# Optimization experiments

Measured on AMD Instinct MI355X. Metric: run time of the kernel, lower is better.

The kernel has to match this reference:

```python
import jax, jax.numpy as jnp
import numpy as np

B, T, I, H = 4096, 512, 3, 64


def setup_inputs() -> dict:
    key = jax.random.key(0)
    ks = jax.random.split(key, 8)
    s = 1.0 / np.sqrt(H)  # PyTorch LSTM init scale
    x = jax.random.normal(ks[0], (B, T, I), dtype=jnp.float32)
    W_ih = jax.random.uniform(ks[1], (4 * H, I), minval=-s, maxval=s, dtype=jnp.float32)
    W_hh = jax.random.uniform(ks[2], (4 * H, H), minval=-s, maxval=s, dtype=jnp.float32)
    b_ih = jax.random.uniform(ks[3], (4 * H,), minval=-s, maxval=s, dtype=jnp.float32)
    b_hh = jax.random.uniform(ks[4], (4 * H,), minval=-s, maxval=s, dtype=jnp.float32)
    W_dec = jax.random.uniform(ks[5], (I, H), minval=-s, maxval=s, dtype=jnp.float32)
    b_dec = jax.random.uniform(ks[6], (I,), minval=-s, maxval=s, dtype=jnp.float32)
    return {"x": x, "W_ih": W_ih, "W_hh": W_hh, "b_ih": b_ih, "b_hh": b_hh,
            "W_dec": W_dec, "b_dec": b_dec}


def _lstm(x, W_ih, W_hh, b_ih, b_hh):
    # Precompute input contribution for all timesteps: [B, T, 4H]
    x_gates = jnp.einsum('bti,gi->btg', x, W_ih) + b_ih + b_hh
    h0 = jnp.zeros((x.shape[0], H), dtype=x.dtype)
    c0 = jnp.zeros((x.shape[0], H), dtype=x.dtype)

    def step(carry, xg_t):
        h, c = carry
        gates = xg_t + h @ W_hh.T  # [B, 4H]
        i_g, f_g, g_g, o_g = jnp.split(gates, 4, axis=-1)  # PyTorch order i,f,g,o
        i_g = jax.nn.sigmoid(i_g)
        f_g = jax.nn.sigmoid(f_g)
        g_g = jnp.tanh(g_g)
        o_g = jax.nn.sigmoid(o_g)
        c_new = f_g * c + i_g * g_g
        h_new = o_g * jnp.tanh(c_new)
        return (h_new, c_new), h_new

    _, hs = jax.lax.scan(step, (h0, c0), jnp.swapaxes(x_gates, 0, 1))  # [T, B, H]
    return jnp.swapaxes(hs, 0, 1)  # [B, T, H]


def reference(x, W_ih, W_hh, b_ih, b_hh, W_dec, b_dec):
    lstm_out = _lstm(x, W_ih, W_hh, b_ih, b_hh)
    return jnp.einsum('bth,oh->bto', lstm_out, W_dec) + b_dec  # [B, T, I]
```

## Files before the change

### kernel.cpp

```cpp
#include <hip/hip_runtime.h>


#define TLEN 512
#define TCHUNK 64
#define ROWS 16

typedef float    float4_t __attribute__((ext_vector_type(4)));
typedef _Float16 halfx8   __attribute__((ext_vector_type(8)));

#define INV2048 4.8828125e-4f

__device__ __forceinline__ float fexp2(float x){ return __builtin_amdgcn_exp2f(x); }
__device__ __forceinline__ float frcp (float x){ return __builtin_amdgcn_rcpf(x); }
__device__ __forceinline__ float sigm (float x){ return frcp(1.f + fexp2(-1.44269504f*x)); }
__device__ __forceinline__ float tanh_(float x){ return 1.f - 2.f*frcp(1.f + fexp2(2.88539008f*x)); }

__device__ __forceinline__ unsigned short hbits(_Float16 h){
  union { _Float16 h; unsigned short u; } x; x.h = h; return x.u;
}

__device__ __forceinline__ void split8h(const float* v, halfx8& hi, halfx8& lo){
  #pragma unroll
  for (int j = 0; j < 8; j++){
    _Float16 h = (_Float16)v[j];
    hi[j] = h;
    lo[j] = (_Float16)((v[j] - (float)h) * 2048.0f);
  }
}

#define MFMA(a,b,c) __builtin_amdgcn_mfma_f32_16x16x32_f16((a),(b),(c),0,0,0)

#define HHI 0
#define HS_SZ 2304
#define XOF 0
#define XPK 3136
#define OOF 7232
#define LF_SZ 10368

__global__ __launch_bounds__(256, 1)
void LSTMAnomalyDetector_kernel(
    const float* __restrict__ x,     const float* __restrict__ W_ih,
    const float* __restrict__ W_hh,  const float* __restrict__ b_ih,
    const float* __restrict__ b_hh,  const float* __restrict__ W_dec,
    const float* __restrict__ b_dec, float* __restrict__ out)
{
  __shared__ __align__(16) unsigned short HS[HS_SZ];
  __shared__ __align__(16) float          LF[LF_SZ];

  const int tid  = threadIdx.x;
  const int w    = tid >> 6;
  const int lane = tid & 63;
  const int q    = lane >> 4;
  const int lid  = lane & 15;
  const int b0   = blockIdx.x * ROWS;
  const int cw   = w*16 + lid;

  halfx8 Bh[4][2], Bl[4][2];
  halfx8 Dh[2],    Dl[2];
  float  wi[4][3], bsum[4];

  #pragma unroll
  for (int tl = 0; tl < 4; tl++){
    const int g = tl*64 + cw;
    #pragma unroll
    for (int kt = 0; kt < 2; kt++){
      const float* p = W_hh + g*64 + kt*32 + q*8;
      float v[8];
      #pragma unroll
      for (int j = 0; j < 8; j++) v[j] = p[j];
      split8h(v, Bh[tl][kt], Bl[tl][kt]);
    }
    wi[tl][0] = W_ih[g*3+0];
    wi[tl][1] = W_ih[g*3+1];
    wi[tl][2] = W_ih[g*3+2];
    bsum[tl]  = b_ih[g] + b_hh[g];
  }
  #pragma unroll
  for (int kt = 0; kt < 2; kt++){
    float v[8] = {0.f,0.f,0.f,0.f,0.f,0.f,0.f,0.f};
    if (lid < 3){
      const float* p = W_dec + lid*64 + kt*32 + q*8;
      #pragma unroll
      for (int j = 0; j < 8; j++) v[j] = p[j];
    }
    split8h(v, Dh[kt], Dl[kt]);
  }
  const float bdec = (lid < 3) ? b_dec[lid] : 0.f;

  halfx8 ah0 = {}, ah1 = {};
  float creg[4] = {0.f, 0.f, 0.f, 0.f};
  float4_t xp4[4];

  auto loadx = [&](int d){
    #pragma unroll
    for (int r = 0; r < 4; r++){
      float4_t xv = *(const float4_t*)&LF[XPK + d*64 + (q*4+r)*4];
      #pragma unroll
      for (int tl = 0; tl < 4; tl++)
        xp4[tl][r] = fmaf(wi[tl][2], xv[2],
                      fmaf(wi[tl][1], xv[1],
                        fmaf(wi[tl][0], xv[0], bsum[tl])));
    }
  };

  #pragma unroll
  for (int s = 0; s < 3; s++){
    const int f = tid + 256*s;
    const int row = f/48; const int off = (f%48)*4;
    float4_t v = *(const float4_t*)(x + (size_t)(b0+row)*1536 + off);
    *(float4_t*)&LF[XOF + row*196 + off] = v;
  }
  __syncthreads();
  #pragma unroll
  for (int s = 0; s < 4; s++){
    const int p = tid + 256*s;
    const float* xr = &LF[XOF + (p & 15)*196 + (p >> 4)*3];
    float4_t v = {xr[0], xr[1], xr[2], 0.f};
    *(float4_t*)&LF[XPK + p*4] = v;
  }
  __syncthreads();
  loadx(0);

  for (int t = 0; t < TLEN; ++t){
    const int dt = t & (TCHUNK-1);
    const int hb = (t & 1) * 1152;

    float4_t c1 = xp4[0];
    c1 = MFMA(ah0, Bh[0][0], c1);
    c1 = MFMA(ah1, Bh[0][1], c1);
    float4_t c2 = {0.f,0.f,0.f,0.f};
    c2 = MFMA(ah0, Bl[0][0], c2);
    c2 = MFMA(ah1, Bl[0][1], c2);
    float4_t g0;
    #pragma unroll
    for (int r = 0; r < 4; r++) g0[r] = fmaf(c2[r], INV2048, c1[r]);
    float4_t ig;
    #pragma unroll
    for (int r = 0; r < 4; r++) ig[r] = sigm(g0[r]);

    c1 = xp4[1];
    c1 = MFMA(ah0, Bh[1][0], c1);
    c1 = MFMA(ah1, Bh[1][1], c1);
    c2 = (float4_t){0.f,0.f,0.f,0.f};
    c2 = MFMA(ah0, Bl[1][0], c2);
    c2 = MFMA(ah1, Bl[1][1], c2);
    float4_t g1;
    #pragma unroll
    for (int r = 0; r < 4; r++) g1[r] = fmaf(c2[r], INV2048, c1[r]);
    float4_t fg;
    #pragma unroll
    for (int r = 0; r < 4; r++) fg[r] = sigm(g1[r]);

    c1 = xp4[2];
    c1 = MFMA(ah0, Bh[2][0], c1);
    c1 = MFMA(ah1, Bh[2][1], c1);
    c2 = (float4_t){0.f,0.f,0.f,0.f};
    c2 = MFMA(ah0, Bl[2][0], c2);
    c2 = MFMA(ah1, Bl[2][1], c2);
    float4_t g2;
    #pragma unroll
    for (int r = 0; r < 4; r++) g2[r] = fmaf(c2[r], INV2048, c1[r]);
    float4_t gg;
    #pragma unroll
    for (int r = 0; r < 4; r++) gg[r] = tanh_(g2[r]);

    c1 = xp4[3];
    c1 = MFMA(ah0, Bh[3][0], c1);
    c1 = MFMA(ah1, Bh[3][1], c1);
    c2 = (float4_t){0.f,0.f,0.f,0.f};
    c2 = MFMA(ah0, Bl[3][0], c2);
    c2 = MFMA(ah1, Bl[3][1], c2);
    float4_t g3;
    #pragma unroll
    for (int r = 0; r < 4; r++) g3[r] = fmaf(c2[r], INV2048, c1[r]);

    #pragma unroll
    for (int r = 0; r < 4; r++){
      const float og = sigm(g3[r]);
      creg[r] = fg[r]*creg[r] + ig[r]*gg[r];
      const float h = og * tanh_(creg[r]);
      const _Float16 h16 = (_Float16)h;
      const int m = q*4 + r;
      HS[HHI + hb + m*72 + cw] = hbits(h16);
    }

    if (dt != TCHUNK-1) loadx(dt+1);

    __syncthreads();

    {
      const unsigned short* ph = &HS[HHI + hb + lid*72 + q*8];
      ah0 = *(const halfx8*)&ph[0];
      ah1 = *(const halfx8*)&ph[32];
    }

    if (w == 0){
      float4_t d1 = {0.f,0.f,0.f,0.f};
      d1 = MFMA(ah0, Dh[0], d1);
      d1 = MFMA(ah1, Dh[1], d1);
      float4_t d2 = {0.f,0.f,0.f,0.f};
      d2 = MFMA(ah0, Dl[0], d2);
      d2 = MFMA(ah1, Dl[1], d2);
      if (lid < 3){
        #pragma unroll
        for (int r = 0; r < 4; r++)
          LF[OOF + (q*4+r)*196 + dt*3 + lid] = fmaf(d2[r], INV2048, d1[r]) + bdec;
      }
    }

    if (dt == TCHUNK-1){
      __syncthreads();
      const int t0 = t - (TCHUNK-1);
      #pragma unroll
      for (int s = 0; s < 3; s++){
        const int f = tid + 256*s;
        const int row = f/48; const int off = (f%48)*4;
        float4_t v = *(const float4_t*)&LF[OOF + row*196 + off];
        *(float4_t*)(out + (size_t)(b0+row)*1536 + t0*3 + off) = v;
      }
      if (t + 1 < TLEN){
        #pragma unroll
        for (int s = 0; s < 3; s++){
          const int f = tid + 256*s;
          const int row = f/48; const int off = (f%48)*4;
          float4_t v = *(const float4_t*)(x + (size_t)(b0+row)*1536 + (t+1)*3 + off);
          *(float4_t*)&LF[XOF + row*196 + off] = v;
        }
        __syncthreads();
        #pragma unroll
        for (int s = 0; s < 4; s++){
          const int p = tid + 256*s;
          const float* xr = &LF[XOF + (p & 15)*196 + (p >> 4)*3];
          float4_t v = {xr[0], xr[1], xr[2], 0.f};
          *(float4_t*)&LF[XPK + p*4] = v;
        }
      }
      __syncthreads();
      if (t + 1 < TLEN) loadx(0);
    }
  }
}

extern "C" void kernel_launch(void* const* d_in, const int* in_sizes, int n_in,
                              void* d_out, int out_size, void* d_ws, size_t ws_size,
                              hipStream_t stream)
{
  const float* x     = (const float*)d_in[0];
  const float* W_ih  = (const float*)d_in[1];
  const float* W_hh  = (const float*)d_in[2];
  const float* b_ih  = (const float*)d_in[3];
  const float* b_hh  = (const float*)d_in[4];
  const float* W_dec = (const float*)d_in[5];
  const float* b_dec = (const float*)d_in[6];
  float* out = (float*)d_out;

  const int B = in_sizes[0] / (TLEN * 3);
  const int blocks = B / ROWS;
  hipLaunchKernelGGL(LSTMAnomalyDetector_kernel, dim3(blocks), dim3(256), 0, stream,
                     x, W_ih, W_hh, b_ih, b_hh, W_dec, b_dec, out);
}
```

Baseline: 485.3 us.

## Rotate decoder MFMA across waves, defer it into next step, drop lo-split

Result: no change. 492.1 us (+1.4%).

```diff
diff --git a/kernel.cpp b/kernel.cpp
--- a/kernel.cpp
+++ b/kernel.cpp
@@ -56,7 +56,7 @@
   const int cw   = w*16 + lid;
 
   halfx8 Bh[4][2], Bl[4][2];
-  halfx8 Dh[2],    Dl[2];
+  halfx8 Dh[2];
   float  wi[4][3], bsum[4];
 
   #pragma unroll
@@ -77,13 +77,13 @@
   }
   #pragma unroll
   for (int kt = 0; kt < 2; kt++){
-    float v[8] = {0.f,0.f,0.f,0.f,0.f,0.f,0.f,0.f};
+    #pragma unroll
+    for (int j = 0; j < 8; j++) Dh[kt][j] = (_Float16)0.f;
     if (lid < 3){
       const float* p = W_dec + lid*64 + kt*32 + q*8;
       #pragma unroll
-      for (int j = 0; j < 8; j++) v[j] = p[j];
-    }
-    split8h(v, Dh[kt], Dl[kt]);
+      for (int j = 0; j < 8; j++) Dh[kt][j] = (_Float16)p[j];
+    }
   }
   const float bdec = (lid < 3) ? b_dec[lid] : 0.f;
 
@@ -138,6 +138,18 @@
     #pragma unroll
     for (int r = 0; r < 4; r++) ig[r] = sigm(g0[r]);
 
+    if (t > 0 && w == ((t-1) & 3)){
+      float4_t d1 = {0.f,0.f,0.f,0.f};
+      d1 = MFMA(ah0, Dh[0], d1);
+      d1 = MFMA(ah1, Dh[1], d1);
+      if (lid < 3){
+        const int dto = (t-1) & (TCHUNK-1);
+        #pragma unroll
+        for (int r = 0; r < 4; r++)
+          LF[OOF + (q*4+r)*196 + dto*3 + lid] = d1[r] + bdec;
+      }
+    }
+
     c1 = xp4[1];
     c1 = MFMA(ah0, Bh[1][0], c1);
     c1 = MFMA(ah1, Bh[1][1], c1);
@@ -194,23 +206,8 @@
       ah1 = *(const halfx8*)&ph[32];
     }
 
-    if (w == 0){
-      float4_t d1 = {0.f,0.f,0.f,0.f};
-      d1 = MFMA(ah0, Dh[0], d1);
-      d1 = MFMA(ah1, Dh[1], d1);
-      float4_t d2 = {0.f,0.f,0.f,0.f};
-      d2 = MFMA(ah0, Dl[0], d2);
-      d2 = MFMA(ah1, Dl[1], d2);
-      if (lid < 3){
-        #pragma unroll
-        for (int r = 0; r < 4; r++)
-          LF[OOF + (q*4+r)*196 + dt*3 + lid] = fmaf(d2[r], INV2048, d1[r]) + bdec;
-      }
-    }
-
-    if (dt == TCHUNK-1){
-      __syncthreads();
-      const int t0 = t - (TCHUNK-1);
+    if (dt == 0 && t > 0){
+      const int t0 = t - TCHUNK;
       #pragma unroll
       for (int s = 0; s < 3; s++){
         const int f = tid + 256*s;
@@ -218,25 +215,49 @@
         float4_t v = *(const float4_t*)&LF[OOF + row*196 + off];
         *(float4_t*)(out + (size_t)(b0+row)*1536 + t0*3 + off) = v;
       }
-      if (t + 1 < TLEN){
-        #pragma unroll
-        for (int s = 0; s < 3; s++){
-          const int f = tid + 256*s;
-          const int row = f/48; const int off = (f%48)*4;
-          float4_t v = *(const float4_t*)(x + (size_t)(b0+row)*1536 + (t+1)*3 + off);
-          *(float4_t*)&LF[XOF + row*196 + off] = v;
-        }
-        __syncthreads();
-        #pragma unroll
-        for (int s = 0; s < 4; s++){
-          const int p = tid + 256*s;
-          const float* xr = &LF[XOF + (p & 15)*196 + (p >> 4)*3];
-          float4_t v = {xr[0], xr[1], xr[2], 0.f};
-          *(float4_t*)&LF[XPK + p*4] = v;
-        }
-      }
       __syncthreads();
-      if (t + 1 < TLEN) loadx(0);
+    }
+
+    if (dt == TCHUNK-1 && t + 1 < TLEN){
+      #pragma unroll
+      for (int s = 0; s < 3; s++){
+        const int f = tid + 256*s;
+        const int row = f/48; const int off = (f%48)*4;
+        float4_t v = *(const float4_t*)(x + (size_t)(b0+row)*1536 + (t+1)*3 + off);
+        *(float4_t*)&LF[XOF + row*196 + off] = v;
+      }
+      __syncthreads();
+      #pragma unroll
+      for (int s = 0; s < 4; s++){
+        const int p = tid + 256*s;
+        const float* xr = &LF[XOF + (p & 15)*196 + (p >> 4)*3];
+        float4_t v = {xr[0], xr[1], xr[2], 0.f};
+        *(float4_t*)&LF[XPK + p*4] = v;
+      }
+      __syncthreads();
+      loadx(0);
+    }
+  }
+
+  if (w == 3){
+    float4_t d1 = {0.f,0.f,0.f,0.f};
+    d1 = MFMA(ah0, Dh[0], d1);
+    d1 = MFMA(ah1, Dh[1], d1);
+    if (lid < 3){
+      #pragma unroll
+      for (int r = 0; r < 4; r++)
+        LF[OOF + (q*4+r)*196 + 63*3 + lid] = d1[r] + bdec;
+    }
+  }
+  __syncthreads();
+  {
+    const int t0 = TLEN - TCHUNK;
+    #pragma unroll
+    for (int s = 0; s < 3; s++){
+      const int f = tid + 256*s;
+      const int row = f/48; const int off = (f%48)*4;
+      float4_t v = *(const float4_t*)&LF[OOF + row*196 + off];
+      *(float4_t*)(out + (size_t)(b0+row)*1536 + t0*3 + off) = v;
     }
   }
 }
```

## Reorder LSTM gate computation, split time loop by chunk, drop decoder lo-split

Applied to the files above, without the earlier changes.

Result: faster. 448.0 us (-7.7%).

```diff
diff --git a/kernel.cpp b/kernel.cpp
--- a/kernel.cpp
+++ b/kernel.cpp
@@ -56,7 +56,7 @@
   const int cw   = w*16 + lid;
 
   halfx8 Bh[4][2], Bl[4][2];
-  halfx8 Dh[2],    Dl[2];
+  halfx8 Dh[2];
   float  wi[4][3], bsum[4];
 
   #pragma unroll
@@ -77,13 +77,13 @@
   }
   #pragma unroll
   for (int kt = 0; kt < 2; kt++){
-    float v[8] = {0.f,0.f,0.f,0.f,0.f,0.f,0.f,0.f};
+    #pragma unroll
+    for (int j = 0; j < 8; j++) Dh[kt][j] = (_Float16)0.f;
     if (lid < 3){
       const float* p = W_dec + lid*64 + kt*32 + q*8;
       #pragma unroll
-      for (int j = 0; j < 8; j++) v[j] = p[j];
-    }
-    split8h(v, Dh[kt], Dl[kt]);
+      for (int j = 0; j < 8; j++) Dh[kt][j] = (_Float16)p[j];
+    }
   }
   const float bdec = (lid < 3) ? b_dec[lid] : 0.f;
 
@@ -103,40 +103,18 @@
     }
   };
 
-  #pragma unroll
-  for (int s = 0; s < 3; s++){
-    const int f = tid + 256*s;
-    const int row = f/48; const int off = (f%48)*4;
-    float4_t v = *(const float4_t*)(x + (size_t)(b0+row)*1536 + off);
-    *(float4_t*)&LF[XOF + row*196 + off] = v;
-  }
-  __syncthreads();
-  #pragma unroll
-  for (int s = 0; s < 4; s++){
-    const int p = tid + 256*s;
-    const float* xr = &LF[XOF + (p & 15)*196 + (p >> 4)*3];
-    float4_t v = {xr[0], xr[1], xr[2], 0.f};
-    *(float4_t*)&LF[XPK + p*4] = v;
-  }
-  __syncthreads();
-  loadx(0);
-
-  for (int t = 0; t < TLEN; ++t){
-    const int dt = t & (TCHUNK-1);
+  auto step = [&](int t, int dt, bool last){
     const int hb = (t & 1) * 1152;
 
-    float4_t c1 = xp4[0];
-    c1 = MFMA(ah0, Bh[0][0], c1);
-    c1 = MFMA(ah1, Bh[0][1], c1);
+    float4_t c1 = xp4[3];
+    c1 = MFMA(ah0, Bh[3][0], c1);
+    c1 = MFMA(ah1, Bh[3][1], c1);
     float4_t c2 = {0.f,0.f,0.f,0.f};
-    c2 = MFMA(ah0, Bl[0][0], c2);
-    c2 = MFMA(ah1, Bl[0][1], c2);
-    float4_t g0;
-    #pragma unroll
-    for (int r = 0; r < 4; r++) g0[r] = fmaf(c2[r], INV2048, c1[r]);
-    float4_t ig;
-    #pragma unroll
-    for (int r = 0; r < 4; r++) ig[r] = sigm(g0[r]);
+    c2 = MFMA(ah0, Bl[3][0], c2);
+    c2 = MFMA(ah1, Bl[3][1], c2);
+    float4_t og;
+    #pragma unroll
+    for (int r = 0; r < 4; r++) og[r] = sigm(fmaf(c2[r], INV2048, c1[r]));
 
     c1 = xp4[1];
     c1 = MFMA(ah0, Bh[1][0], c1);
@@ -144,12 +122,22 @@
     c2 = (float4_t){0.f,0.f,0.f,0.f};
     c2 = MFMA(ah0, Bl[1][0], c2);
     c2 = MFMA(ah1, Bl[1][1], c2);
-    float4_t g1;
-    #pragma unroll
-    for (int r = 0; r < 4; r++) g1[r] = fmaf(c2[r], INV2048, c1[r]);
-    float4_t fg;
-    #pragma unroll
-    for (int r = 0; r < 4; r++) fg[r] = sigm(g1[r]);
+    float4_t cp;
+    #pragma unroll
+    for (int r = 0; r < 4; r++){
+      const float fg = sigm(fmaf(c2[r], INV2048, c1[r]));
+      cp[r] = fg * creg[r];
+    }
+
+    c1 = xp4[0];
+    c1 = MFMA(ah0, Bh[0][0], c1);
+    c1 = MFMA(ah1, Bh[0][1], c1);
+    c2 = (float4_t){0.f,0.f,0.f,0.f};
+    c2 = MFMA(ah0, Bl[0][0], c2);
+    c2 = MFMA(ah1, Bl[0][1], c2);
+    float4_t ig;
+    #pragma unroll
+    for (int r = 0; r < 4; r++) ig[r] = sigm(fmaf(c2[r], INV2048, c1[r]));
 
     c1 = xp4[2];
     c1 = MFMA(ah0, Bh[2][0], c1);
@@ -157,34 +145,16 @@
     c2 = (float4_t){0.f,0.f,0.f,0.f};
     c2 = MFMA(ah0, Bl[2][0], c2);
     c2 = MFMA(ah1, Bl[2][1], c2);
-    float4_t g2;
-    #pragma unroll
-    for (int r = 0; r < 4; r++) g2[r] = fmaf(c2[r], INV2048, c1[r]);
-    float4_t gg;
-    #pragma unroll
-    for (int r = 0; r < 4; r++) gg[r] = tanh_(g2[r]);
-
-    c1 = xp4[3];
-    c1 = MFMA(ah0, Bh[3][0], c1);
-    c1 = MFMA(ah1, Bh[3][1], c1);
-    c2 = (float4_t){0.f,0.f,0.f,0.f};
-    c2 = MFMA(ah0, Bl[3][0], c2);
-    c2 = MFMA(ah1, Bl[3][1], c2);
-    float4_t g3;
-    #pragma unroll
-    for (int r = 0; r < 4; r++) g3[r] = fmaf(c2[r], INV2048, c1[r]);
-
     #pragma unroll
     for (int r = 0; r < 4; r++){
-      const float og = sigm(g3[r]);
-      creg[r] = fg[r]*creg[r] + ig[r]*gg[r];
-      const float h = og * tanh_(creg[r]);
+      const float gg = tanh_(fmaf(c2[r], INV2048, c1[r]));
+      creg[r] = fmaf(ig[r], gg, cp[r]);
+      const float h = og[r] * tanh_(creg[r]);
       const _Float16 h16 = (_Float16)h;
-      const int m = q*4 + r;
-      HS[HHI + hb + m*72 + cw] = hbits(h16);
-    }
-
-    if (dt != TCHUNK-1) loadx(dt+1);
+      HS[HHI + hb + (q*4+r)*72 + cw] = hbits(h16);
+    }
+
+    if (!last) loadx(dt+1);
 
     __syncthreads();
 
@@ -198,46 +168,68 @@
       float4_t d1 = {0.f,0.f,0.f,0.f};
       d1 = MFMA(ah0, Dh[0], d1);
       d1 = MFMA(ah1, Dh[1], d1);
-      float4_t d2 = {0.f,0.f,0.f,0.f};
-      d2 = MFMA(ah0, Dl[0], d2);
-      d2 = MFMA(ah1, Dl[1], d2);
       if (lid < 3){
         #pragma unroll
         for (int r = 0; r < 4; r++)
-          LF[OOF + (q*4+r)*196 + dt*3 + lid] = fmaf(d2[r], INV2048, d1[r]) + bdec;
+          LF[OOF + (q*4+r)*196 + dt*3 + lid] = d1[r] + bdec;
       }
     }
-
-    if (dt == TCHUNK-1){
-      __syncthreads();
-      const int t0 = t - (TCHUNK-1);
+  };
+
+  #pragma unroll
+  for (int s = 0; s < 3; s++){
+    const int f = tid + 256*s;
+    const int row = f/48; const int off = (f%48)*4;
+    float4_t v = *(const float4_t*)(x + (size_t)(b0+row)*1536 + off);
+    *(float4_t*)&LF[XOF + row*196 + off] = v;
+  }
+  __syncthreads();
+  #pragma unroll
+  for (int s = 0; s < 4; s++){
+    const int p = tid + 256*s;
+    const float* xr = &LF[XOF + (p & 15)*196 + (p >> 4)*3];
+    float4_t v = {xr[0], xr[1], xr[2], 0.f};
+    *(float4_t*)&LF[XPK + p*4] = v;
+  }
+  __syncthreads();
+  loadx(0);
+
+  for (int ck = 0; ck < TLEN/TCHUNK; ++ck){
+    const int tb = ck * TCHUNK;
+
+    for (int dt = 0; dt < TCHUNK-1; ++dt)
+      step(tb + dt, dt, false);
+
+    step(tb + TCHUNK-1, TCHUNK-1, true);
+
+    __syncthreads();
+    #pragma unroll
+    for (int s = 0; s < 3; s++){
+      const int f = tid + 256*s;
+      const int row = f/48; const int off = (f%48)*4;
+      float4_t v = *(const float4_t*)&LF[OOF + row*196 + off];
+      *(float4_t*)(out + (size_t)(b0+row)*1536 + tb*3 + off) = v;
+    }
+    if (ck + 1 < TLEN/TCHUNK){
+      const int tn = tb + TCHUNK;
       #pragma unroll
       for (int s = 0; s < 3; s++){
         const int f = tid + 256*s;
         const int row = f/48; const int off = (f%48)*4;
-        float4_t v = *(const float4_t*)&LF[OOF + row*196 + off];
-        *(float4_t*)(out + (size_t)(b0+row)*1536 + t0*3 + off) = v;
-      }
-      if (t + 1 < TLEN){
-        #pragma unroll
-        for (int s = 0; s < 3; s++){
-          const int f = tid + 256*s;
-          const int row = f/48; const int off = (f%48)*4;
-          float4_t v = *(const float4_t*)(x + (size_t)(b0+row)*1536 + (t+1)*3 + off);
-          *(float4_t*)&LF[XOF + row*196 + off] = v;
-        }
-        __syncthreads();
-        #pragma unroll
-        for (int s = 0; s < 4; s++){
-          const int p = tid + 256*s;
-          const float* xr = &LF[XOF + (p & 15)*196 + (p >> 4)*3];
-          float4_t v = {xr[0], xr[1], xr[2], 0.f};
-          *(float4_t*)&LF[XPK + p*4] = v;
-        }
+        float4_t v = *(const float4_t*)(x + (size_t)(b0+row)*1536 + tn*3 + off);
+        *(float4_t*)&LF[XOF + row*196 + off] = v;
       }
       __syncthreads();
-      if (t + 1 < TLEN) loadx(0);
-    }
+      #pragma unroll
+      for (int s = 0; s < 4; s++){
+        const int p = tid + 256*s;
+        const float* xr = &LF[XOF + (p & 15)*196 + (p >> 4)*3];
+        float4_t v = {xr[0], xr[1], xr[2], 0.f};
+        *(float4_t*)&LF[XPK + p*4] = v;
+      }
+    }
+    __syncthreads();
+    if (ck + 1 < TLEN/TCHUNK) loadx(0);
   }
 }
 
```
